# Performance work log

Measured on AMD Instinct MI355X. Metric: run time of the kernel, lower is better.

## Reference

```python
import jax, jax.numpy as jnp
import numpy as np

B, T, CH, V, E, L = 64, 1024, 256, 32000, 64, 128  # batch, enc_len, channel, vocab, emb_dim, latent_dims


def setup_inputs() -> dict:
    key = jax.random.key(0)
    ks = jax.random.split(key, 13)
    s = 0.05  # weight init scale
    return {
        "prev_cont_vec": jax.random.normal(ks[0], (B, CH), jnp.float32),
        "F": jax.random.normal(ks[1], (B, T, CH), jnp.float32),
        "prev_char": jax.random.normal(ks[2], (B, V), jnp.float32),
        "state_h": jax.random.normal(ks[3], (B, L), jnp.float32),
        "state_c": jax.random.normal(ks[4], (B, L), jnp.float32),
        # learned parameters (all Dense layers use_bias=False)
        "Wc": jax.random.normal(ks[5], (V, E), jnp.float32) * s,
        "Wct1": jax.random.normal(ks[6], (CH, E), jnp.float32) * s,
        "Wo": jax.random.normal(ks[7], (L, V), jnp.float32) * s,
        "Wct2": jax.random.normal(ks[8], (CH, V), jnp.float32) * s,
        "lstm_kernel": jax.random.normal(ks[9], (E, 4 * L), jnp.float32) * s,
        "lstm_recurrent": jax.random.normal(ks[10], (L, 4 * L), jnp.float32) * s,
        "W_h": jax.random.normal(ks[11], (L, CH), jnp.float32) * s,
        "V_attn": jax.random.normal(ks[12], (1, 1, CH), jnp.float32) * s,
    }


def reference(prev_cont_vec, F, prev_char, state_h, state_c,
              Wc, Wct1, Wo, Wct2, lstm_kernel, lstm_recurrent, W_h, V_attn):
    # lstm input: Wc(prev_char) + Wct1(prev_cont_vec)  -> [B, E]
    lstm_inp = prev_char @ Wc + prev_cont_vec @ Wct1
    # Keras LSTMCell (no bias), gate order i, f, c, o
    z = lstm_inp @ lstm_kernel + state_h @ lstm_recurrent  # [B, 4L]
    zi, zf, zg, zo = jnp.split(z, 4, axis=-1)
    i = jax.nn.sigmoid(zi)
    f = jax.nn.sigmoid(zf)
    g = jnp.tanh(zg)
    o = jax.nn.sigmoid(zo)
    new_c = f * state_c + i * g
    new_h = o * jnp.tanh(new_c)
    # training=True branch: clip returned cell state
    new_c_out = jnp.clip(new_c, -10.0, 10.0)
    # additive attention over time axis of F [B, T, CH]
    H_tfm = (new_h @ W_h)[:, None, :]            # [B, 1, CH]
    e_t = V_attn * jnp.tanh(H_tfm + F)           # [B, T, CH]
    attn = jax.nn.softmax(e_t, axis=1)           # softmax over T, per channel
    c_t = jnp.sum(attn * F, axis=1)              # [B, CH]
    # output distribution
    O_t = jax.nn.softmax(new_h @ Wo + c_t @ Wct2, axis=1)  # [B, V]
    return (O_t, c_t, new_h, new_c_out)
```

## Files before the change

kernel.cpp:

```cpp
#include <hip/hip_runtime.h>
#include <hip/hip_bf16.h>

#define BB 64
#define TT 1024
#define CHN 256
#define VV 32000
#define EE 64
#define LL 128
#define NC1 250
#define KC1 128
#define TS 16

typedef unsigned short u16;
typedef unsigned int u32;
typedef __attribute__((ext_vector_type(8))) short short8;
typedef __attribute__((ext_vector_type(16))) float f32x16;

__device__ __forceinline__ float fast_rcp(float x) { return __builtin_amdgcn_rcpf(x); }
__device__ __forceinline__ float tanh_fast(float y) {
    float e = __expf(2.0f * y);
    return 1.0f - 2.0f * fast_rcp(1.0f + e);
}
__device__ __forceinline__ float sigmoid_fast(float x) {
    return fast_rcp(1.0f + __expf(-x));
}
__device__ __forceinline__ u16 f2bf(float f) {
    u32 u = __float_as_uint(f);
    return (u16)((u + 0x7fffu + ((u >> 16) & 1u)) >> 16);
}
__device__ __forceinline__ u32 pack_bf2(float lo, float hi) {
    return (u32)f2bf(lo) | ((u32)f2bf(hi) << 16);
}
__device__ __forceinline__ float bf2f(u16 x) {
    return __uint_as_float(((u32)x) << 16);
}
__device__ __forceinline__ size_t apk_idx(int g, int b) {
    return ((size_t)(((g >> 3) * 2 + ((g & 7) >> 2)) * 64 + b)) * 4 + (g & 3);
}

__global__ __launch_bounds__(256) void k1_stage1(const float* __restrict__ A,
                                                 const float* __restrict__ Wc,
                                                 float* __restrict__ part) {
    __shared__ float sW[KC1][EE];
    __shared__ float sAT[KC1][32];
    const int kc = blockIdx.x;
    const int k0 = kc * KC1;
    const int y  = blockIdx.y;
    const int t  = threadIdx.x;

    #pragma unroll
    for (int f = t; f < 2048; f += 256)
        *(float4*)(&sW[0][0] + f * 4) = *(const float4*)(Wc + (size_t)k0 * EE + f * 4);
    {
        const int bl = t & 31;
        const int kq = t >> 5;
        const float* src = A + (size_t)(y * 32 + bl) * VV + k0 + kq * 16;
        #pragma unroll
        for (int j4 = 0; j4 < 4; ++j4) {
            float4 v = *(const float4*)(src + j4 * 4);
            sAT[kq * 16 + j4 * 4 + 0][bl] = v.x;
            sAT[kq * 16 + j4 * 4 + 1][bl] = v.y;
            sAT[kq * 16 + j4 * 4 + 2][bl] = v.z;
            sAT[kq * 16 + j4 * 4 + 3][bl] = v.w;
        }
    }
    __syncthreads();

    const int e  = t & 63;
    const int b0 = (t >> 6) * 8;
    float acc[8];
    #pragma unroll
    for (int i = 0; i < 8; ++i) acc[i] = 0.0f;

    #pragma unroll 4
    for (int k = 0; k < KC1; ++k) {
        float wt = sW[k][e];
        float4 a0 = *(const float4*)&sAT[k][b0];
        float4 a1 = *(const float4*)&sAT[k][b0 + 4];
        acc[0] = fmaf(a0.x, wt, acc[0]);
        acc[1] = fmaf(a0.y, wt, acc[1]);
        acc[2] = fmaf(a0.z, wt, acc[2]);
        acc[3] = fmaf(a0.w, wt, acc[3]);
        acc[4] = fmaf(a1.x, wt, acc[4]);
        acc[5] = fmaf(a1.y, wt, acc[5]);
        acc[6] = fmaf(a1.z, wt, acc[6]);
        acc[7] = fmaf(a1.w, wt, acc[7]);
    }
    const int gb = y * 32 + b0;
    #pragma unroll
    for (int i = 0; i < 8; ++i)
        part[((size_t)(gb + i) * NC1 + kc) * EE + e] = acc[i];
}

__global__ __launch_bounds__(512) void k2_lstm(const float* __restrict__ part,
    const float* __restrict__ pcv, const float* __restrict__ state_h,
    const float* __restrict__ state_c, const float* __restrict__ Wct1,
    const float* __restrict__ lstm_kernel, const float* __restrict__ lstm_rec,
    const float* __restrict__ W_h,
    float* __restrict__ out_newh, float* __restrict__ out_newc,
    u32* __restrict__ Apk, float* __restrict__ Htfm) {
    __shared__ float red[8][EE];
    __shared__ float inp[EE];
    __shared__ float sh[LL];
    __shared__ float z[4 * LL];
    __shared__ float nh[LL];
    const int b = blockIdx.x;
    const int t = threadIdx.x;
    const int e  = t & 63;
    const int g  = t >> 6;

    {
        float s = 0.0f;
        #pragma unroll 4
        for (int j = g; j < NC1; j += 8)
            s += part[((size_t)b * NC1 + j) * EE + e];
        const int c0 = g * 32;
        #pragma unroll 8
        for (int c = 0; c < 32; ++c)
            s = fmaf(pcv[b * CHN + c0 + c], Wct1[(size_t)(c0 + c) * EE + e], s);
        red[g][e] = s;
    }
    __syncthreads();
    if (t < EE) {
        float s = 0.0f;
        #pragma unroll
        for (int j = 0; j < 8; ++j) s += red[j][t];
        inp[t] = s;
    } else if (t >= 64 && t < 64 + LL) {
        sh[t - 64] = state_h[b * LL + (t - 64)];
    }
    __syncthreads();
    {
        float a = 0.0f;
        #pragma unroll 8
        for (int e2 = 0; e2 < EE; ++e2) a = fmaf(inp[e2], lstm_kernel[e2 * 512 + t], a);
        #pragma unroll 8
        for (int l = 0; l < LL; ++l) a = fmaf(sh[l], lstm_rec[l * 512 + t], a);
        z[t] = a;
    }
    __syncthreads();
    if (t < LL) {
        float zi = z[t], zf = z[LL + t], zg = z[2 * LL + t], zo = z[3 * LL + t];
        float ig = sigmoid_fast(zi);
        float fg = sigmoid_fast(zf);
        float gg = tanh_fast(zg);
        float og = sigmoid_fast(zo);
        float co = state_c[b * LL + t];
        float cn = fg * co + ig * gg;
        float hn = og * tanh_fast(cn);
        out_newc[b * LL + t] = fminf(fmaxf(cn, -10.0f), 10.0f);
        out_newh[b * LL + t] = hn;
        nh[t] = hn;
    }
    __syncthreads();
    if (t < CHN) {
        float a = 0.0f;
        #pragma unroll 8
        for (int l = 0; l < LL; ++l) a = fmaf(nh[l], W_h[l * CHN + t], a);
        Htfm[b * CHN + t] = a;
    } else if (t >= CHN && t < CHN + 64) {
        const int gp = t - CHN;
        Apk[apk_idx(gp, b)] = pack_bf2(nh[2 * gp], nh[2 * gp + 1]);
    }
}

__global__ __launch_bounds__(256) void k3_attn(const float* __restrict__ F,
    const float* __restrict__ Htfm, const float* __restrict__ Vattn,
    float* __restrict__ pS, float* __restrict__ pW) {
    __shared__ float4 sS[256];
    __shared__ float4 sW[256];
    const int b    = blockIdx.x;
    const int ts   = blockIdx.y;
    const int lane = threadIdx.x & 63;
    const int w    = threadIdx.x >> 6;
    const int ch   = lane * 4;

    float4 h = *(const float4*)(Htfm + b * CHN + ch);
    float4 v = *(const float4*)(Vattn + ch);
    float s0 = 0, s1 = 0, s2 = 0, s3 = 0;
    float a0 = 0, a1 = 0, a2 = 0, a3 = 0;

    const float* Fp = F + ((size_t)b * TT + ts * (TT / TS) + w * 16) * CHN + ch;
    float4 cur = *(const float4*)(Fp);
    #pragma unroll
    for (int t = 0; t < 16; ++t) {
        float4 nxt;
        if (t < 15) nxt = *(const float4*)(Fp + (size_t)(t + 1) * CHN);
        float e0 = __expf(v.x * tanh_fast(h.x + cur.x));
        float e1 = __expf(v.y * tanh_fast(h.y + cur.y));
        float e2 = __expf(v.z * tanh_fast(h.z + cur.z));
        float e3 = __expf(v.w * tanh_fast(h.w + cur.w));
        s0 += e0; s1 += e1; s2 += e2; s3 += e3;
        a0 = fmaf(e0, cur.x, a0); a1 = fmaf(e1, cur.y, a1);
        a2 = fmaf(e2, cur.z, a2); a3 = fmaf(e3, cur.w, a3);
        cur = nxt;
    }
    sS[threadIdx.x] = make_float4(s0, s1, s2, s3);
    sW[threadIdx.x] = make_float4(a0, a1, a2, a3);
    __syncthreads();
    if (threadIdx.x < 64) {
        float4 S = sS[threadIdx.x];
        float4 W = sW[threadIdx.x];
        #pragma unroll
        for (int j = 1; j < 4; ++j) {
            float4 s = sS[j * 64 + threadIdx.x];
            float4 q = sW[j * 64 + threadIdx.x];
            S.x += s.x; S.y += s.y; S.z += s.z; S.w += s.w;
            W.x += q.x; W.y += q.y; W.z += q.z; W.w += q.w;
        }
        int base = (b * TS + ts) * CHN + threadIdx.x * 4;
        *(float4*)(pS + base) = S;
        *(float4*)(pW + base) = W;
    }
}

__global__ __launch_bounds__(256) void k4_combine(const float* __restrict__ pS,
    const float* __restrict__ pW, float* __restrict__ out_ct, u32* __restrict__ Apk) {
    __shared__ float sc[CHN];
    const int b = blockIdx.x;
    const int ch = threadIdx.x;
    float S = 0.0f, W = 0.0f;
    #pragma unroll
    for (int j = 0; j < TS; ++j) {
        int idx = (b * TS + j) * CHN + ch;
        S += pS[idx];
        W += pW[idx];
    }
    float c = W / S;
    out_ct[b * CHN + ch] = c;
    sc[ch] = c;
    __syncthreads();
    if (ch < 128)
        Apk[apk_idx(64 + ch, b)] = pack_bf2(sc[2 * ch], sc[2 * ch + 1]);
}

__global__ __launch_bounds__(256) void k5_logits(const float* __restrict__ Wo,
    const float* __restrict__ Wct2, const u32* __restrict__ Apk,
    u16* __restrict__ expb, float* __restrict__ psum) {
    __shared__ float rp[4][32];
    const int t    = threadIdx.x;
    const int lane = t & 63;
    const int wv   = t >> 6;
    const int m    = lane & 31;
    const int kq   = lane >> 5;
    const int y    = blockIdx.y;
    const int n0   = blockIdx.x * 128 + wv * 32;
    const int gb0  = y * 32;

    uint4 af[24];
    #pragma unroll
    for (int tt = 0; tt < 24; ++tt)
        af[tt] = *(const uint4*)&Apk[((size_t)((tt * 2 + kq) * 64) + gb0 + m) * 4];

    f32x16 acc = {0.0f, 0.0f, 0.0f, 0.0f, 0.0f, 0.0f, 0.0f, 0.0f,
                  0.0f, 0.0f, 0.0f, 0.0f, 0.0f, 0.0f, 0.0f, 0.0f};

    float wbuf[2][8];
    {
        const float* c0 = Wo + (size_t)(kq * 8) * VV + n0 + m;
        #pragma unroll
        for (int j = 0; j < 8; ++j) wbuf[0][j] = c0[(size_t)j * VV];
    }

    #pragma unroll
    for (int tt = 0; tt < 24; ++tt) {
        if (tt < 23) {
            const int kn = (tt + 1) * 16 + kq * 8;
            const float* cn = (kn < LL ? Wo + (size_t)kn * VV
                                       : Wct2 + (size_t)(kn - LL) * VV) + n0 + m;
            #pragma unroll
            for (int j = 0; j < 8; ++j) wbuf[(tt + 1) & 1][j] = cn[(size_t)j * VV];
        }
        short8 a, b;
        u32 ax = af[tt].x, ay = af[tt].y, az = af[tt].z, aw = af[tt].w;
        #pragma unroll
        for (int r = 0; r < 4; ++r) {
            u32 lo = __float_as_uint(wbuf[tt & 1][2 * r]);
            u32 hi = __float_as_uint(wbuf[tt & 1][2 * r + 1]);
            u32 bp = (lo >> 16) | (hi & 0xffff0000u);
            u32 ap = (r == 0) ? ax : (r == 1) ? ay : (r == 2) ? az : aw;
            a[2 * r]     = (short)(ap & 0xffff);
            a[2 * r + 1] = (short)(ap >> 16);
            b[2 * r]     = (short)(bp & 0xffff);
            b[2 * r + 1] = (short)(bp >> 16);
        }
        acc = __builtin_amdgcn_mfma_f32_32x32x16_bf16(a, b, acc, 0, 0, 0);
    }

    float ex[16];
    #pragma unroll
    for (int r = 0; r < 16; ++r) {
        const int row = (r & 3) + 8 * (r >> 2) + 4 * kq;
        ex[r] = __expf(acc[r]);
        expb[(size_t)(gb0 + row) * VV + n0 + m] = f2bf(ex[r]);
    }
    #pragma unroll
    for (int r = 0; r < 16; ++r) {
        float s = ex[r];
        s += __shfl_xor(s, 1, 64);  s += __shfl_xor(s, 2, 64);
        s += __shfl_xor(s, 4, 64);  s += __shfl_xor(s, 8, 64);
        s += __shfl_xor(s, 16, 64);
        ex[r] = s;
    }
    if (m == 0) {
        #pragma unroll
        for (int r = 0; r < 16; ++r)
            rp[wv][(r & 3) + 8 * (r >> 2) + 4 * kq] = ex[r];
    }
    __syncthreads();
    if (t < 32)
        psum[(size_t)blockIdx.x * BB + gb0 + t] =
            rp[0][t] + rp[1][t] + rp[2][t] + rp[3][t];
}

__global__ __launch_bounds__(256) void k5c_norm(const u16* __restrict__ expb,
    const float* __restrict__ psum, float* __restrict__ O) {
    __shared__ float red[256];
    const int b   = blockIdx.x;
    const int seg = blockIdx.y;
    const int t   = threadIdx.x;

    red[t] = (t < NC1) ? psum[(size_t)t * BB + b] : 0.0f;
    __syncthreads();
    #pragma unroll
    for (int off = 128; off > 0; off >>= 1) {
        if (t < off) red[t] += red[t + off];
        __syncthreads();
    }
    const float inv = fast_rcp(red[0]);

    const u16* src = expb + (size_t)b * VV + seg * 8000;
    float* dst     = O + (size_t)b * VV + seg * 8000;
    #pragma unroll 2
    for (int i = t; i < 2000; i += 256) {
        uint2 pk = *(const uint2*)(src + i * 4);
        float4 f;
        f.x = bf2f((u16)(pk.x & 0xffff)) * inv;
        f.y = bf2f((u16)(pk.x >> 16)) * inv;
        f.z = bf2f((u16)(pk.y & 0xffff)) * inv;
        f.w = bf2f((u16)(pk.y >> 16)) * inv;
        *(float4*)(dst + i * 4) = f;
    }
}

extern "C" void kernel_launch(void* const* d_in, const int* in_sizes, int n_in,
                              void* d_out, int out_size, void* d_ws, size_t ws_size,
                              hipStream_t stream) {
    (void)in_sizes; (void)n_in; (void)out_size; (void)ws_size;
    const float* pcv       = (const float*)d_in[0];
    const float* F         = (const float*)d_in[1];
    const float* prev_char = (const float*)d_in[2];
    const float* state_h   = (const float*)d_in[3];
    const float* state_c   = (const float*)d_in[4];
    const float* Wc        = (const float*)d_in[5];
    const float* Wct1      = (const float*)d_in[6];
    const float* Wo        = (const float*)d_in[7];
    const float* Wct2      = (const float*)d_in[8];
    const float* lstm_k    = (const float*)d_in[9];
    const float* lstm_r    = (const float*)d_in[10];
    const float* W_h       = (const float*)d_in[11];
    const float* Vattn     = (const float*)d_in[12];

    float* outO  = (float*)d_out;
    float* outCt = outO + (size_t)BB * VV;
    float* outH  = outCt + (size_t)BB * CHN;
    float* outC  = outH + (size_t)BB * LL;

    float* ws     = (float*)d_ws;
    float* part   = ws;
    float* pS     = part + (size_t)NC1 * BB * EE;
    float* pW     = pS + (size_t)BB * TS * CHN;
    float* Htfm   = pW + (size_t)BB * TS * CHN;
    float* psum   = Htfm + (size_t)BB * CHN;
    u32*   Apk    = (u32*)(psum + (size_t)NC1 * BB);
    u16*   expb   = (u16*)(Apk + 12288);

    hipLaunchKernelGGL(k1_stage1, dim3(NC1, 2), dim3(256), 0, stream, prev_char, Wc, part);
    hipLaunchKernelGGL(k2_lstm, dim3(BB), dim3(512), 0, stream, part, pcv, state_h,
                       state_c, Wct1, lstm_k, lstm_r, W_h, outH, outC, Apk, Htfm);
    hipLaunchKernelGGL(k3_attn, dim3(BB, TS), dim3(256), 0, stream, F, Htfm, Vattn, pS, pW);
    hipLaunchKernelGGL(k4_combine, dim3(BB), dim3(256), 0, stream, pS, pW, outCt, Apk);
    hipLaunchKernelGGL(k5_logits, dim3(NC1, 2), dim3(256), 0, stream, Wo, Wct2, Apk, expb, psum);
    hipLaunchKernelGGL(k5c_norm, dim3(BB, 4), dim3(256), 0, stream, expb, psum, outO);
}
```

Measured before the change: 221.4 us.

## Rebalance grids: merge batch halves, split attention time finer, deepen prefetch

k1 now covers all 64 batch rows per block with 512 threads, so each Wc chunk is loaded once instead of twice. k3 splits the time axis into 32 segments of 8 steps to get more blocks. k5 gives each block 64 vocab columns across both batch halves, so each Wo/Wct2 column is read once per block, and uses a three-deep register prefetch. k5c uses more segments and reduces 500 partial sums. The cost is larger workspace partials, a bigger k4 combine and more register pressure in k5.

```diff
diff --git a/kernel.cpp b/kernel.cpp
--- a/kernel.cpp
+++ b/kernel.cpp
@@ -9,7 +9,8 @@
 #define LL 128
 #define NC1 250
 #define KC1 128
-#define TS 16
+#define TS 32
+#define NV5 500
 
 typedef unsigned short u16;
 typedef unsigned int u32;
@@ -38,23 +39,22 @@
     return ((size_t)(((g >> 3) * 2 + ((g & 7) >> 2)) * 64 + b)) * 4 + (g & 3);
 }
 
-__global__ __launch_bounds__(256) void k1_stage1(const float* __restrict__ A,
+__global__ __launch_bounds__(512) void k1_stage1(const float* __restrict__ A,
                                                  const float* __restrict__ Wc,
                                                  float* __restrict__ part) {
     __shared__ float sW[KC1][EE];
-    __shared__ float sAT[KC1][32];
+    __shared__ float sAT[KC1][64];
     const int kc = blockIdx.x;
     const int k0 = kc * KC1;
-    const int y  = blockIdx.y;
     const int t  = threadIdx.x;
 
     #pragma unroll
-    for (int f = t; f < 2048; f += 256)
+    for (int f = t; f < 2048; f += 512)
         *(float4*)(&sW[0][0] + f * 4) = *(const float4*)(Wc + (size_t)k0 * EE + f * 4);
     {
-        const int bl = t & 31;
-        const int kq = t >> 5;
-        const float* src = A + (size_t)(y * 32 + bl) * VV + k0 + kq * 16;
+        const int bl = t & 63;
+        const int kq = t >> 6;
+        const float* src = A + (size_t)bl * VV + k0 + kq * 16;
         #pragma unroll
         for (int j4 = 0; j4 < 4; ++j4) {
             float4 v = *(const float4*)(src + j4 * 4);
@@ -86,10 +86,9 @@
         acc[6] = fmaf(a1.z, wt, acc[6]);
         acc[7] = fmaf(a1.w, wt, acc[7]);
     }
-    const int gb = y * 32 + b0;
     #pragma unroll
     for (int i = 0; i < 8; ++i)
-        part[((size_t)(gb + i) * NC1 + kc) * EE + e] = acc[i];
+        part[((size_t)(b0 + i) * NC1 + kc) * EE + e] = acc[i];
 }
 
 __global__ __launch_bounds__(512) void k2_lstm(const float* __restrict__ part,
@@ -180,12 +179,12 @@
     float s0 = 0, s1 = 0, s2 = 0, s3 = 0;
     float a0 = 0, a1 = 0, a2 = 0, a3 = 0;
 
-    const float* Fp = F + ((size_t)b * TT + ts * (TT / TS) + w * 16) * CHN + ch;
+    const float* Fp = F + ((size_t)b * TT + ts * (TT / TS) + w * 8) * CHN + ch;
     float4 cur = *(const float4*)(Fp);
     #pragma unroll
-    for (int t = 0; t < 16; ++t) {
+    for (int t = 0; t < 8; ++t) {
         float4 nxt;
-        if (t < 15) nxt = *(const float4*)(Fp + (size_t)(t + 1) * CHN);
+        if (t < 7) nxt = *(const float4*)(Fp + (size_t)(t + 1) * CHN);
         float e0 = __expf(v.x * tanh_fast(h.x + cur.x));
         float e1 = __expf(v.y * tanh_fast(h.y + cur.y));
         float e2 = __expf(v.z * tanh_fast(h.z + cur.z));
@@ -243,9 +242,9 @@
     const int wv   = t >> 6;
     const int m    = lane & 31;
     const int kq   = lane >> 5;
-    const int y    = blockIdx.y;
-    const int n0   = blockIdx.x * 128 + wv * 32;
-    const int gb0  = y * 32;
+    const int vt   = blockIdx.x;
+    const int n0   = vt * 64 + (wv >> 1) * 32;
+    const int gb0  = (wv & 1) * 32;
 
     uint4 af[24];
     #pragma unroll
@@ -255,28 +254,29 @@
     f32x16 acc = {0.0f, 0.0f, 0.0f, 0.0f, 0.0f, 0.0f, 0.0f, 0.0f,
                   0.0f, 0.0f, 0.0f, 0.0f, 0.0f, 0.0f, 0.0f, 0.0f};
 
-    float wbuf[2][8];
-    {
-        const float* c0 = Wo + (size_t)(kq * 8) * VV + n0 + m;
-        #pragma unroll
-        for (int j = 0; j < 8; ++j) wbuf[0][j] = c0[(size_t)j * VV];
+    float wbuf[3][8];
+    #pragma unroll
+    for (int pf = 0; pf < 2; ++pf) {
+        const float* c0 = Wo + (size_t)(pf * 16 + kq * 8) * VV + n0 + m;
+        #pragma unroll
+        for (int j = 0; j < 8; ++j) wbuf[pf][j] = c0[(size_t)j * VV];
     }
 
     #pragma unroll
     for (int tt = 0; tt < 24; ++tt) {
-        if (tt < 23) {
-            const int kn = (tt + 1) * 16 + kq * 8;
+        if (tt < 22) {
+            const int kn = (tt + 2) * 16 + kq * 8;
             const float* cn = (kn < LL ? Wo + (size_t)kn * VV
                                        : Wct2 + (size_t)(kn - LL) * VV) + n0 + m;
             #pragma unroll
-            for (int j = 0; j < 8; ++j) wbuf[(tt + 1) & 1][j] = cn[(size_t)j * VV];
+            for (int j = 0; j < 8; ++j) wbuf[(tt + 2) % 3][j] = cn[(size_t)j * VV];
         }
         short8 a, b;
         u32 ax = af[tt].x, ay = af[tt].y, az = af[tt].z, aw = af[tt].w;
         #pragma unroll
         for (int r = 0; r < 4; ++r) {
-            u32 lo = __float_as_uint(wbuf[tt & 1][2 * r]);
-            u32 hi = __float_as_uint(wbuf[tt & 1][2 * r + 1]);
+            u32 lo = __float_as_uint(wbuf[tt % 3][2 * r]);
+            u32 hi = __float_as_uint(wbuf[tt % 3][2 * r + 1]);
             u32 bp = (lo >> 16) | (hi & 0xffff0000u);
             u32 ap = (r == 0) ? ax : (r == 1) ? ay : (r == 2) ? az : aw;
             a[2 * r]     = (short)(ap & 0xffff);
@@ -308,9 +308,10 @@
             rp[wv][(r & 3) + 8 * (r >> 2) + 4 * kq] = ex[r];
     }
     __syncthreads();
-    if (t < 32)
-        psum[(size_t)blockIdx.x * BB + gb0 + t] =
-            rp[0][t] + rp[1][t] + rp[2][t] + rp[3][t];
+    if (t < 64) {
+        const int hb = t >> 5, r = t & 31;
+        psum[(size_t)vt * BB + t] = rp[hb][r] + rp[2 + hb][r];
+    }
 }
 
 __global__ __launch_bounds__(256) void k5c_norm(const u16* __restrict__ expb,
@@ -320,7 +321,9 @@
     const int seg = blockIdx.y;
     const int t   = threadIdx.x;
 
-    red[t] = (t < NC1) ? psum[(size_t)t * BB + b] : 0.0f;
+    float s = psum[(size_t)t * BB + b];
+    if (t + 256 < NV5) s += psum[(size_t)(t + 256) * BB + b];
+    red[t] = s;
     __syncthreads();
     #pragma unroll
     for (int off = 128; off > 0; off >>= 1) {
@@ -329,10 +332,10 @@
     }
     const float inv = fast_rcp(red[0]);
 
-    const u16* src = expb + (size_t)b * VV + seg * 8000;
-    float* dst     = O + (size_t)b * VV + seg * 8000;
+    const u16* src = expb + (size_t)b * VV + seg * 4000;
+    float* dst     = O + (size_t)b * VV + seg * 4000;
     #pragma unroll 2
-    for (int i = t; i < 2000; i += 256) {
+    for (int i = t; i < 1000; i += 256) {
         uint2 pk = *(const uint2*)(src + i * 4);
         float4 f;
         f.x = bf2f((u16)(pk.x & 0xffff)) * inv;
@@ -372,14 +375,14 @@
     float* pW     = pS + (size_t)BB * TS * CHN;
     float* Htfm   = pW + (size_t)BB * TS * CHN;
     float* psum   = Htfm + (size_t)BB * CHN;
-    u32*   Apk    = (u32*)(psum + (size_t)NC1 * BB);
+    u32*   Apk    = (u32*)(psum + (size_t)NV5 * BB);
     u16*   expb   = (u16*)(Apk + 12288);
 
-    hipLaunchKernelGGL(k1_stage1, dim3(NC1, 2), dim3(256), 0, stream, prev_char, Wc, part);
+    hipLaunchKernelGGL(k1_stage1, dim3(NC1), dim3(512), 0, stream, prev_char, Wc, part);
     hipLaunchKernelGGL(k2_lstm, dim3(BB), dim3(512), 0, stream, part, pcv, state_h,
                        state_c, Wct1, lstm_k, lstm_r, W_h, outH, outC, Apk, Htfm);
     hipLaunchKernelGGL(k3_attn, dim3(BB, TS), dim3(256), 0, stream, F, Htfm, Vattn, pS, pW);
     hipLaunchKernelGGL(k4_combine, dim3(BB), dim3(256), 0, stream, pS, pW, outCt, Apk);
-    hipLaunchKernelGGL(k5_logits, dim3(NC1, 2), dim3(256), 0, stream, Wo, Wct2, Apk, expb, psum);
-    hipLaunchKernelGGL(k5c_norm, dim3(BB, 4), dim3(256), 0, stream, expb, psum, outO);
-}
+    hipLaunchKernelGGL(k5_logits, dim3(NV5), dim3(256), 0, stream, Wo, Wct2, Apk, expb, psum);
+    hipLaunchKernelGGL(k5c_norm, dim3(BB, 8), dim3(256), 0, stream, expb, psum, outO);
+}
```

New measurement: 226.2 us. +2.2%, slower.

## Fuse attention combine into attn kernel via atomics; deepen logits prefetch

Applied to the files above, without the earlier changes.

Removes the separate k4_combine launch. Each attention block now atomically adds its per-channel partial sums into per-batch accumulators, and the last-arriving block, found through a counter, computes c_t and packs it for the logits GEMM. Accumulators and counters are zeroed in the LSTM kernel. The attention loop now issues four F loads at a time, and the logits kernel prefetches weights two steps ahead with a triple buffer. This trades one kernel launch and the partial-buffer round trip for float atomics, whose summation order is nondeterministic, and for extra register pressure.

```diff
diff --git a/kernel.cpp b/kernel.cpp
--- a/kernel.cpp
+++ b/kernel.cpp
@@ -98,7 +98,8 @@
     const float* __restrict__ lstm_kernel, const float* __restrict__ lstm_rec,
     const float* __restrict__ W_h,
     float* __restrict__ out_newh, float* __restrict__ out_newc,
-    u32* __restrict__ Apk, float* __restrict__ Htfm) {
+    u32* __restrict__ Apk, float* __restrict__ Htfm,
+    float* __restrict__ accS, float* __restrict__ accW, u32* __restrict__ cnt) {
     __shared__ float red[8][EE];
     __shared__ float inp[EE];
     __shared__ float sh[LL];
@@ -108,6 +109,12 @@
     const int t = threadIdx.x;
     const int e  = t & 63;
     const int g  = t >> 6;
+
+    if (t < CHN) {
+        accS[b * CHN + t] = 0.0f;
+        accW[b * CHN + t] = 0.0f;
+    }
+    if (t == 511) cnt[b] = 0u;
 
     {
         float s = 0.0f;
@@ -166,13 +173,16 @@
 
 __global__ __launch_bounds__(256) void k3_attn(const float* __restrict__ F,
     const float* __restrict__ Htfm, const float* __restrict__ Vattn,
-    float* __restrict__ pS, float* __restrict__ pW) {
+    float* __restrict__ accS, float* __restrict__ accW, u32* __restrict__ cnt,
+    float* __restrict__ out_ct, u32* __restrict__ Apk) {
     __shared__ float4 sS[256];
     __shared__ float4 sW[256];
+    __shared__ int lastFlag;
     const int b    = blockIdx.x;
     const int ts   = blockIdx.y;
-    const int lane = threadIdx.x & 63;
-    const int w    = threadIdx.x >> 6;
+    const int tid  = threadIdx.x;
+    const int lane = tid & 63;
+    const int w    = tid >> 6;
     const int ch   = lane * 4;
 
     float4 h = *(const float4*)(Htfm + b * CHN + ch);
@@ -180,58 +190,66 @@
     float s0 = 0, s1 = 0, s2 = 0, s3 = 0;
     float a0 = 0, a1 = 0, a2 = 0, a3 = 0;
 
-    const float* Fp = F + ((size_t)b * TT + ts * (TT / TS) + w * 16) * CHN + ch;
-    float4 cur = *(const float4*)(Fp);
-    #pragma unroll
-    for (int t = 0; t < 16; ++t) {
-        float4 nxt;
-        if (t < 15) nxt = *(const float4*)(Fp + (size_t)(t + 1) * CHN);
-        float e0 = __expf(v.x * tanh_fast(h.x + cur.x));
-        float e1 = __expf(v.y * tanh_fast(h.y + cur.y));
-        float e2 = __expf(v.z * tanh_fast(h.z + cur.z));
-        float e3 = __expf(v.w * tanh_fast(h.w + cur.w));
-        s0 += e0; s1 += e1; s2 += e2; s3 += e3;
-        a0 = fmaf(e0, cur.x, a0); a1 = fmaf(e1, cur.y, a1);
-        a2 = fmaf(e2, cur.z, a2); a3 = fmaf(e3, cur.w, a3);
-        cur = nxt;
-    }
-    sS[threadIdx.x] = make_float4(s0, s1, s2, s3);
-    sW[threadIdx.x] = make_float4(a0, a1, a2, a3);
-    __syncthreads();
-    if (threadIdx.x < 64) {
-        float4 S = sS[threadIdx.x];
-        float4 W = sW[threadIdx.x];
+    const float* Fp = F + ((size_t)b * TT + ts * 64 + w * 16) * CHN + ch;
+    #pragma unroll
+    for (int q = 0; q < 16; q += 4) {
+        float4 c0 = *(const float4*)(Fp + (size_t)(q + 0) * CHN);
+        float4 c1 = *(const float4*)(Fp + (size_t)(q + 1) * CHN);
+        float4 c2 = *(const float4*)(Fp + (size_t)(q + 2) * CHN);
+        float4 c3 = *(const float4*)(Fp + (size_t)(q + 3) * CHN);
+        #pragma unroll
+        for (int j = 0; j < 4; ++j) {
+            float4 cu = (j == 0) ? c0 : (j == 1) ? c1 : (j == 2) ? c2 : c3;
+            float e0 = __expf(v.x * tanh_fast(h.x + cu.x));
+            float e1 = __expf(v.y * tanh_fast(h.y + cu.y));
+            float e2 = __expf(v.z * tanh_fast(h.z + cu.z));
+            float e3 = __expf(v.w * tanh_fast(h.w + cu.w));
+            s0 += e0; s1 += e1; s2 += e2; s3 += e3;
+            a0 = fmaf(e0, cu.x, a0); a1 = fmaf(e1, cu.y, a1);
+            a2 = fmaf(e2, cu.z, a2); a3 = fmaf(e3, cu.w, a3);
+        }
+    }
+    sS[tid] = make_float4(s0, s1, s2, s3);
+    sW[tid] = make_float4(a0, a1, a2, a3);
+    __syncthreads();
+    if (tid < 64) {
+        float4 S = sS[tid];
+        float4 W = sW[tid];
         #pragma unroll
         for (int j = 1; j < 4; ++j) {
-            float4 s = sS[j * 64 + threadIdx.x];
-            float4 q = sW[j * 64 + threadIdx.x];
+            float4 s = sS[j * 64 + tid];
+            float4 q = sW[j * 64 + tid];
             S.x += s.x; S.y += s.y; S.z += s.z; S.w += s.w;
             W.x += q.x; W.y += q.y; W.z += q.z; W.w += q.w;
         }
-        int base = (b * TS + ts) * CHN + threadIdx.x * 4;
-        *(float4*)(pS + base) = S;
-        *(float4*)(pW + base) = W;
-    }
-}
-
-__global__ __launch_bounds__(256) void k4_combine(const float* __restrict__ pS,
-    const float* __restrict__ pW, float* __restrict__ out_ct, u32* __restrict__ Apk) {
-    __shared__ float sc[CHN];
-    const int b = blockIdx.x;
-    const int ch = threadIdx.x;
-    float S = 0.0f, W = 0.0f;
-    #pragma unroll
-    for (int j = 0; j < TS; ++j) {
-        int idx = (b * TS + j) * CHN + ch;
-        S += pS[idx];
-        W += pW[idx];
-    }
-    float c = W / S;
-    out_ct[b * CHN + ch] = c;
-    sc[ch] = c;
-    __syncthreads();
-    if (ch < 128)
-        Apk[apk_idx(64 + ch, b)] = pack_bf2(sc[2 * ch], sc[2 * ch + 1]);
+        const int base = b * CHN + tid * 4;
+        atomicAdd(&accS[base + 0], S.x);
+        atomicAdd(&accS[base + 1], S.y);
+        atomicAdd(&accS[base + 2], S.z);
+        atomicAdd(&accS[base + 3], S.w);
+        atomicAdd(&accW[base + 0], W.x);
+        atomicAdd(&accW[base + 1], W.y);
+        atomicAdd(&accW[base + 2], W.z);
+        atomicAdd(&accW[base + 3], W.w);
+    }
+    __threadfence();
+    __syncthreads();
+    if (tid == 0) {
+        u32 old = atomicAdd(&cnt[b], 1u);
+        lastFlag = (old == TS - 1) ? 1 : 0;
+    }
+    __syncthreads();
+    if (lastFlag) {
+        float* sc = (float*)sS;
+        float S = atomicAdd(&accS[b * CHN + tid], 0.0f);
+        float W = atomicAdd(&accW[b * CHN + tid], 0.0f);
+        float c = W / S;
+        out_ct[b * CHN + tid] = c;
+        sc[tid] = c;
+        __syncthreads();
+        if (tid < 128)
+            Apk[apk_idx(64 + tid, b)] = pack_bf2(sc[2 * tid], sc[2 * tid + 1]);
+    }
 }
 
 __global__ __launch_bounds__(256) void k5_logits(const float* __restrict__ Wo,
@@ -255,28 +273,29 @@
     f32x16 acc = {0.0f, 0.0f, 0.0f, 0.0f, 0.0f, 0.0f, 0.0f, 0.0f,
                   0.0f, 0.0f, 0.0f, 0.0f, 0.0f, 0.0f, 0.0f, 0.0f};
 
-    float wbuf[2][8];
-    {
-        const float* c0 = Wo + (size_t)(kq * 8) * VV + n0 + m;
-        #pragma unroll
-        for (int j = 0; j < 8; ++j) wbuf[0][j] = c0[(size_t)j * VV];
+    float wbuf[3][8];
+    #pragma unroll
+    for (int pf = 0; pf < 2; ++pf) {
+        const float* c0 = Wo + (size_t)(pf * 16 + kq * 8) * VV + n0 + m;
+        #pragma unroll
+        for (int j = 0; j < 8; ++j) wbuf[pf][j] = c0[(size_t)j * VV];
     }
 
     #pragma unroll
     for (int tt = 0; tt < 24; ++tt) {
-        if (tt < 23) {
-            const int kn = (tt + 1) * 16 + kq * 8;
+        if (tt < 22) {
+            const int kn = (tt + 2) * 16 + kq * 8;
             const float* cn = (kn < LL ? Wo + (size_t)kn * VV
                                        : Wct2 + (size_t)(kn - LL) * VV) + n0 + m;
             #pragma unroll
-            for (int j = 0; j < 8; ++j) wbuf[(tt + 1) & 1][j] = cn[(size_t)j * VV];
+            for (int j = 0; j < 8; ++j) wbuf[(tt + 2) % 3][j] = cn[(size_t)j * VV];
         }
         short8 a, b;
         u32 ax = af[tt].x, ay = af[tt].y, az = af[tt].z, aw = af[tt].w;
         #pragma unroll
         for (int r = 0; r < 4; ++r) {
-            u32 lo = __float_as_uint(wbuf[tt & 1][2 * r]);
-            u32 hi = __float_as_uint(wbuf[tt & 1][2 * r + 1]);
+            u32 lo = __float_as_uint(wbuf[tt % 3][2 * r]);
+            u32 hi = __float_as_uint(wbuf[tt % 3][2 * r + 1]);
             u32 bp = (lo >> 16) | (hi & 0xffff0000u);
             u32 ap = (r == 0) ? ax : (r == 1) ? ay : (r == 2) ? az : aw;
             a[2 * r]     = (short)(ap & 0xffff);
@@ -368,18 +387,20 @@
 
     float* ws     = (float*)d_ws;
     float* part   = ws;
-    float* pS     = part + (size_t)NC1 * BB * EE;
-    float* pW     = pS + (size_t)BB * TS * CHN;
-    float* Htfm   = pW + (size_t)BB * TS * CHN;
+    float* accS   = part + (size_t)NC1 * BB * EE;
+    float* accW   = accS + (size_t)BB * CHN;
+    float* Htfm   = accW + (size_t)BB * CHN;
     float* psum   = Htfm + (size_t)BB * CHN;
-    u32*   Apk    = (u32*)(psum + (size_t)NC1 * BB);
+    u32*   cnt    = (u32*)(psum + (size_t)NC1 * BB);
+    u32*   Apk    = (u32*)(cnt + 64);
     u16*   expb   = (u16*)(Apk + 12288);
 
     hipLaunchKernelGGL(k1_stage1, dim3(NC1, 2), dim3(256), 0, stream, prev_char, Wc, part);
     hipLaunchKernelGGL(k2_lstm, dim3(BB), dim3(512), 0, stream, part, pcv, state_h,
-                       state_c, Wct1, lstm_k, lstm_r, W_h, outH, outC, Apk, Htfm);
-    hipLaunchKernelGGL(k3_attn, dim3(BB, TS), dim3(256), 0, stream, F, Htfm, Vattn, pS, pW);
-    hipLaunchKernelGGL(k4_combine, dim3(BB), dim3(256), 0, stream, pS, pW, outCt, Apk);
+                       state_c, Wct1, lstm_k, lstm_r, W_h, outH, outC, Apk, Htfm,
+                       accS, accW, cnt);
+    hipLaunchKernelGGL(k3_attn, dim3(BB, TS), dim3(256), 0, stream, F, Htfm, Vattn,
+                       accS, accW, cnt, outCt, Apk);
     hipLaunchKernelGGL(k5_logits, dim3(NC1, 2), dim3(256), 0, stream, Wo, Wct2, Apk, expb, psum);
     hipLaunchKernelGGL(k5c_norm, dim3(BB, 4), dim3(256), 0, stream, expb, psum, outO);
 }
```

Result: slower. 322.6 us (+45.7%).
